# Kernel optimization log

Hardware: AMD Instinct MI355X
Metric: run time of the kernel (lower is better)

## Reference

```python
import jax, jax.numpy as jnp
import numpy as np

DT = 0.5
DX = 0.01
MU_UP = 4e-05
PAD = 3  # 7x7 kernel // 2

_LAP = np.array([[0, 0, 0, 2, 0, 0, 0],
                 [0, 0, 0, -27, 0, 0, 0],
                 [0, 0, 0, 270, 0, 0, 0],
                 [2, -27, 270, -980, 270, -27, 2],
                 [0, 0, 0, 270, 0, 0, 0],
                 [0, 0, 0, -27, 0, 0, 0],
                 [0, 0, 0, 2, 0, 0, 0]], dtype=np.float32)
LAP_W = jnp.asarray(_LAP / (DX * DX) / 180.0)[None, None]  # [1,1,7,7]


def _laplace(x):
    # x: [B,1,H,W]; circular padding then valid conv (matches padding_mode='circular')
    xp = jnp.pad(x, ((0, 0), (0, 0), (PAD, PAD), (PAD, PAD)), mode='wrap')
    return jax.lax.conv_general_dilated(xp, LAP_W, (1, 1), 'VALID',
                                        dimension_numbers=('NCHW', 'OIHW', 'NCHW'))


def setup_inputs() -> dict:
    key = jax.random.key(0)
    ks = jax.random.split(key, 7)
    h = jax.random.uniform(ks[0], (16, 2, 1024, 1024), dtype=jnp.float32)
    CA = jax.random.uniform(ks[1], (), dtype=jnp.float32) - 0.5  # ~ -rand()+0.5
    CB = jax.random.uniform(ks[2], (), dtype=jnp.float32) - 0.5
    NA = -jax.random.uniform(ks[3], (), dtype=jnp.float32)
    NB = jax.random.uniform(ks[4], (), dtype=jnp.float32)
    f = 0.1 * jax.random.uniform(ks[5], (), dtype=jnp.float32)
    k = 0.1 * jax.random.uniform(ks[6], (), dtype=jnp.float32)
    return {"h": h, "CA": CA, "CB": CB, "NA": NA, "NB": NB, "f": f, "k": k}


def reference(h, CA, CB, NA, NB, f, k):
    mu_u = MU_UP * jax.nn.sigmoid(CA)
    mu_v = MU_UP * jax.nn.sigmoid(CB)

    def f_rhs(u, v):
        uv2 = u * v * v
        f_u = mu_u * _laplace(u) + NA * uv2 + f * (1.0 - u)
        f_v = mu_v * _laplace(v) + NB * uv2 - (k + f) * v
        return f_u, f_v

    u0 = h[:, 0:1]
    v0 = h[:, 1:2]
    k1_u, k1_v = f_rhs(u0, v0)
    k2_u, k2_v = f_rhs(u0 + k1_u * (DT / 2.0), v0 + k1_v * (DT / 2.0))
    k3_u, k3_v = f_rhs(u0 + k2_u * (DT / 2.0), v0 + k2_v * (DT / 2.0))
    k4_u, k4_v = f_rhs(u0 + k3_u * DT, v0 + k3_v * DT)
    u_next = u0 + DT * (k1_u + 2.0 * k2_u + 2.0 * k3_u + k4_u) / 6.0
    v_next = v0 + DT * (k1_v + 2.0 * k2_v + 2.0 * k3_v + k4_v) / 6.0
    return jnp.concatenate((u_next, v_next), axis=1)
```

## Files before the change

### kernel.cpp

```cpp
#include <hip/hip_runtime.h>


typedef float f2 __attribute__((ext_vector_type(2)));
typedef float f4 __attribute__((ext_vector_type(4)));

#define HROWS 64
#define NT    512
#define STEPS (HROWS + 24)

#define W0 ((-980.0f / 1e-4f) / 180.0f)
#define W1 ((  270.0f / 1e-4f) / 180.0f)
#define W2 (( -27.0f / 1e-4f) / 180.0f)
#define W3 ((   2.0f / 1e-4f) / 180.0f)

__device__ __forceinline__ f2 sp(float s) { f2 r; r.x = s; r.y = s; return r; }
__device__ __forceinline__ f2 pfma(float s, f2 a, f2 c) {
    return __builtin_elementwise_fma(sp(s), a, c);
}
__device__ __forceinline__ f2 lo2(f4 a) { return __builtin_shufflevector(a, a, 0, 1); }
__device__ __forceinline__ f2 hi2(f4 a) { return __builtin_shufflevector(a, a, 2, 3); }
__device__ __forceinline__ f4 cat(f2 a, f2 b) { return __builtin_shufflevector(a, b, 0, 1, 2, 3); }

struct Hq  { f2 m2, m1, p1, p2; };
struct Hq4 { f4 m2, m1, p1, p2; };

__device__ __forceinline__ Hq4 rdq4(const f4* __restrict__ L,
                                    int xm2, int xm1, int xp1, int xp2) {
    Hq4 q;
    q.m2 = L[xm2]; q.m1 = L[xm1]; q.p1 = L[xp1]; q.p2 = L[xp2];
    return q;
}

__device__ __forceinline__ void evalp7(f2 w0, f2 w1, f2 w2, f2 w3, f2 w4,
                                       f2 w5, f2 w6, const Hq& q,
                                       f2& lap, f2& ctr)
{
    ctr = w3;
    f2 vp = pfma(W1, w2 + w4, pfma(W2, w1 + w5, sp(W3) * (w0 + w6)));
    f2 m1 = __builtin_shufflevector(q.m1, ctr, 1, 2);
    f2 p1 = __builtin_shufflevector(ctr, q.p1, 1, 2);
    f2 m3 = __builtin_shufflevector(q.m2, q.m1, 1, 2);
    f2 p3 = __builtin_shufflevector(q.p1, q.p2, 1, 2);
    f2 hp = pfma(W1, m1 + p1, pfma(W2, q.m1 + q.p1, sp(W3) * (m3 + p3)));
    lap = pfma(W0, ctr, hp + vp);
}

__global__ __launch_bounds__(NT, 1) void rcnn_rk4_march(
    const float* __restrict__ h,
    const float* __restrict__ pCA, const float* __restrict__ pCB,
    const float* __restrict__ pNA, const float* __restrict__ pNB,
    const float* __restrict__ pf,  const float* __restrict__ pk,
    float* __restrict__ out)
{
    __shared__ f4 S[4][4][NT];

    const int tid = threadIdx.x;
    const int Y0  = blockIdx.x * HROWS;
    const int b   = blockIdx.z;

    const float NA = pNA[0], NB = pNB[0];
    const float ff = pf[0];
    const float kpf = pk[0] + pf[0];
    const float mu_u = 4e-5f / (1.0f + expf(-pCA[0]));
    const float mu_v = 4e-5f / (1.0f + expf(-pCB[0]));

    const size_t baseU = (size_t)b * 2u * 1048576u;
    const size_t baseV = baseU + 1048576u;
    const float* hU = h + baseU + 2 * tid;
    const float* hV = h + baseV + 2 * tid;
    float* oU = out + baseU + 2 * tid;
    float* oV = out + baseV + 2 * tid;

    const int xm2 = (tid - 2) & 511;
    const int xm1 = (tid - 1) & 511;
    const int xp1 = (tid + 1) & 511;
    const int xp2 = (tid + 2) & 511;

    f2 Uu[8], Uv[8], Du[8], Dv[8];
    f2 Y1u[8], Y1v[8], Y2u[8], Y2v[8], Y3u[8], Y3v[8];
    f2 ACu[8], ACv[8];

    const f2 z = sp(0.0f);
    #pragma unroll
    for (int j = 0; j < 8; ++j) {
        Uu[j]=z; Uv[j]=z; Du[j]=z; Dv[j]=z;
        Y1u[j]=z; Y1v[j]=z; Y2u[j]=z; Y2v[j]=z; Y3u[j]=z; Y3v[j]=z;
        ACu[j]=z; ACv[j]=z;
    }

    f2 pAu, pAv, pBu, pBv;
    {
        int r0 = (Y0 - 12) & 1023;
        int r1 = (Y0 - 11) & 1023;
        pAu = *(const f2*)(hU + (size_t)r0 * 1024);
        pAv = *(const f2*)(hV + (size_t)r0 * 1024);
        pBu = *(const f2*)(hU + (size_t)r1 * 1024);
        pBv = *(const f2*)(hV + (size_t)r1 * 1024);
    }

#define STEP(c, G1, G2, G3, G4, tb_)                                          \
  {                                                                           \
    const int t_ = (tb_) + (c);                                               \
                             \
    Du[(c)&7] = Uu[((c)+3)&7]; Dv[(c)&7] = Uv[((c)+3)&7];                     \
                                             \
    Uu[(c)&7] = ((c)&1) ? pBu : pAu;                                          \
    Uv[(c)&7] = ((c)&1) ? pBv : pAv;                                          \
                          \
    S[0][(c)&3][tid] = cat(Uu[((c)+7)&7], Uv[((c)+7)&7]);                     \
                                             \
    {                                                                         \
      int yn = (Y0 - 10 + t_) & 1023;                                         \
      f2 au = *(const f2*)(hU + (size_t)yn * 1024);                           \
      f2 av = *(const f2*)(hV + (size_t)yn * 1024);                           \
      if ((c)&1) { pBu = au; pBv = av; } else { pAu = au; pAv = av; }         \
    }                                                                         \
    if (G1) {                                         \
      Hq4 q = rdq4(&S[0][((c)+2)&3][0], xm2, xm1, xp1, xp2);                  \
      Hq qu = { lo2(q.m2), lo2(q.m1), lo2(q.p1), lo2(q.p2) };                 \
      Hq qv = { hi2(q.m2), hi2(q.m1), hi2(q.p1), hi2(q.p2) };                 \
      f2 lU, cU, lV, cV;                                                      \
      evalp7(Uu[((c)+2)&7], Uu[((c)+3)&7], Uu[((c)+4)&7], Uu[((c)+5)&7],      \
             Uu[((c)+6)&7], Uu[((c)+7)&7], Uu[(c)&7], qu, lU, cU);            \
      evalp7(Uv[((c)+2)&7], Uv[((c)+3)&7], Uv[((c)+4)&7], Uv[((c)+5)&7],      \
             Uv[((c)+6)&7], Uv[((c)+7)&7], Uv[(c)&7], qv, lV, cV);            \
      f2 uv2 = cU * cV * cV;                                                  \
      f2 kU = pfma(mu_u, lU, pfma(NA, uv2, pfma(-ff, cU, sp(ff))));           \
      f2 kV = pfma(mu_v, lV, pfma(NB, uv2, sp(-kpf) * cV));                   \
      Y1u[(c)&7] = pfma(0.25f, kU, cU);                                       \
      Y1v[(c)&7] = pfma(0.25f, kV, cV);                                       \
      S[1][(c)&3][tid] = cat(Y1u[((c)+7)&7], Y1v[((c)+7)&7]);                 \
    }                                                                         \
    if (G2) {                               \
      Hq4 q = rdq4(&S[1][((c)+2)&3][0], xm2, xm1, xp1, xp2);                  \
      Hq qu = { lo2(q.m2), lo2(q.m1), lo2(q.p1), lo2(q.p2) };                 \
      Hq qv = { hi2(q.m2), hi2(q.m1), hi2(q.p1), hi2(q.p2) };                 \
      f2 lU, cU, lV, cV;                                                      \
      evalp7(Y1u[((c)+2)&7], Y1u[((c)+3)&7], Y1u[((c)+4)&7], Y1u[((c)+5)&7],  \
             Y1u[((c)+6)&7], Y1u[((c)+7)&7], Y1u[(c)&7], qu, lU, cU);         \
      evalp7(Y1v[((c)+2)&7], Y1v[((c)+3)&7], Y1v[((c)+4)&7], Y1v[((c)+5)&7],  \
             Y1v[((c)+6)&7], Y1v[((c)+7)&7], Y1v[(c)&7], qv, lV, cV);         \
      f2 uv2 = cU * cV * cV;                                                  \
      f2 kU = pfma(mu_u, lU, pfma(NA, uv2, pfma(-ff, cU, sp(ff))));           \
      f2 kV = pfma(mu_v, lV, pfma(NB, uv2, sp(-kpf) * cV));                   \
      f2 bu = Du[((c)+7)&7], bv = Dv[((c)+7)&7];                \
      f2 nu = pfma(0.25f, kU, bu), nv = pfma(0.25f, kV, bv);                  \
      Y2u[(c)&7] = nu; Y2v[(c)&7] = nv;                                       \
      f2 aU = pfma(4.0f, Y1u[((c)+5)&7], sp(8.0f) * nu);                      \
      f2 aV = pfma(4.0f, Y1v[((c)+5)&7], sp(8.0f) * nv);                      \
      ACu[(c)&7] = pfma(-4.0f, bu, aU);                                       \
      ACv[(c)&7] = pfma(-4.0f, bv, aV);                                       \
      S[2][(c)&3][tid] = cat(Y2u[((c)+7)&7], Y2v[((c)+7)&7]);                 \
    }                                                                         \
    if (G3) {                                         \
      Hq4 q = rdq4(&S[2][((c)+2)&3][0], xm2, xm1, xp1, xp2);                  \
      Hq qu = { lo2(q.m2), lo2(q.m1), lo2(q.p1), lo2(q.p2) };                 \
      Hq qv = { hi2(q.m2), hi2(q.m1), hi2(q.p1), hi2(q.p2) };                 \
      f2 lU, cU, lV, cV;                                                      \
      evalp7(Y2u[((c)+2)&7], Y2u[((c)+3)&7], Y2u[((c)+4)&7], Y2u[((c)+5)&7],  \
             Y2u[((c)+6)&7], Y2u[((c)+7)&7], Y2u[(c)&7], qu, lU, cU);         \
      evalp7(Y2v[((c)+2)&7], Y2v[((c)+3)&7], Y2v[((c)+4)&7], Y2v[((c)+5)&7],  \
             Y2v[((c)+6)&7], Y2v[((c)+7)&7], Y2v[(c)&7], qv, lV, cV);         \
      f2 uv2 = cU * cV * cV;                                                  \
      f2 kU = pfma(mu_u, lU, pfma(NA, uv2, pfma(-ff, cU, sp(ff))));           \
      f2 kV = pfma(mu_v, lV, pfma(NB, uv2, sp(-kpf) * cV));                   \
      Y3u[(c)&7] = pfma(0.5f, kU, Du[((c)+4)&7]);               \
      Y3v[(c)&7] = pfma(0.5f, kV, Dv[((c)+4)&7]);                             \
      S[3][(c)&3][tid] = cat(Y3u[((c)+7)&7], Y3v[((c)+7)&7]);                 \
    }                                                                         \
    if (G4) {                         \
      Hq4 q = rdq4(&S[3][((c)+2)&3][0], xm2, xm1, xp1, xp2);                  \
      Hq qu = { lo2(q.m2), lo2(q.m1), lo2(q.p1), lo2(q.p2) };                 \
      Hq qv = { hi2(q.m2), hi2(q.m1), hi2(q.p1), hi2(q.p2) };                 \
      f2 lU, cU4, lV, cV4;                                                    \
      evalp7(Y3u[((c)+2)&7], Y3u[((c)+3)&7], Y3u[((c)+4)&7], Y3u[((c)+5)&7],  \
             Y3u[((c)+6)&7], Y3u[((c)+7)&7], Y3u[(c)&7], qu, lU, cU4);        \
      evalp7(Y3v[((c)+2)&7], Y3v[((c)+3)&7], Y3v[((c)+4)&7], Y3v[((c)+5)&7],  \
             Y3v[((c)+6)&7], Y3v[((c)+7)&7], Y3v[(c)&7], qv, lV, cV4);        \
      f2 uv2 = cU4 * cV4 * cV4;                                               \
      f2 kU = pfma(mu_u, lU, pfma(NA, uv2, pfma(-ff, cU4, sp(ff))));          \
      f2 kV = pfma(mu_v, lV, pfma(NB, uv2, sp(-kpf) * cV4));                  \
      f2 sU = pfma(4.0f, cU4, kU) + ACu[((c)+2)&7];             \
      f2 sV = pfma(4.0f, cV4, kV) + ACv[((c)+2)&7];                           \
      f2 oUq = sp(1.0f / 12.0f) * sU;                                         \
      f2 oVq = sp(1.0f / 12.0f) * sV;                                         \
      int yS = Y0 + t_ - 24;                                                  \
      *(f2*)(oU + (size_t)yS * 1024) = oUq;                                   \
      *(f2*)(oV + (size_t)yS * 1024) = oVq;                                   \
    }                                                                         \
    if ((c) & 1) {                                                            \
      asm volatile("s_waitcnt lgkmcnt(0)" ::: "memory");                      \
      __builtin_amdgcn_s_barrier();                                           \
    }                                                                         \
  }

    STEP(0,0,0,0,0, 0) STEP(1,0,0,0,0, 0) STEP(2,0,0,0,0, 0) STEP(3,0,0,0,0, 0)
    STEP(4,0,0,0,0, 0) STEP(5,0,0,0,0, 0) STEP(6,1,0,0,0, 0) STEP(7,1,0,0,0, 0)

    STEP(0,1,0,0,0, 8) STEP(1,1,0,0,0, 8) STEP(2,1,0,0,0, 8) STEP(3,1,0,0,0, 8)
    STEP(4,1,1,0,0, 8) STEP(5,1,1,0,0, 8) STEP(6,1,1,0,0, 8) STEP(7,1,1,0,0, 8)

    STEP(0,1,1,0,0,16) STEP(1,1,1,0,0,16) STEP(2,1,1,1,0,16) STEP(3,1,1,1,0,16)
    STEP(4,1,1,1,0,16) STEP(5,1,1,1,0,16) STEP(6,1,1,1,0,16) STEP(7,1,1,1,0,16)

    #pragma unroll 1
    for (int tb = 24; tb < STEPS; tb += 8) {
        STEP(0,1,1,1,1,tb) STEP(1,1,1,1,1,tb) STEP(2,1,1,1,1,tb) STEP(3,1,1,1,1,tb)
        STEP(4,1,1,1,1,tb) STEP(5,1,1,1,1,tb) STEP(6,1,1,1,1,tb) STEP(7,1,1,1,1,tb)
    }
#undef STEP
}

extern "C" void kernel_launch(void* const* d_in, const int* in_sizes, int n_in,
                              void* d_out, int out_size, void* d_ws, size_t ws_size,
                              hipStream_t stream) {
    const float* h   = (const float*)d_in[0];
    const float* pCA = (const float*)d_in[1];
    const float* pCB = (const float*)d_in[2];
    const float* pNA = (const float*)d_in[3];
    const float* pNB = (const float*)d_in[4];
    const float* pf  = (const float*)d_in[5];
    const float* pk  = (const float*)d_in[6];
    float* outp = (float*)d_out;

    dim3 grid(1024 / HROWS, 1, 16);
    dim3 block(NT);
    rcnn_rk4_march<<<grid, block, 0, stream>>>(h, pCA, pCB, pNA, pNB, pf, pk, outp);
}
```

Measured before the change: 90.44 us.

## Read stage-1 horizontal halo from global memory instead of shared memory

The first RK stage no longer writes the input rows to shared memory and reads neighbours back. Each thread instead loads unaligned float4 windows around its columns straight from global (served from cache), two rows ahead, with special handling for the circular wrap at the row ends. This frees one of the four LDS stage buffers and removes one LDS write/read round per row. In exchange it adds extra global loads, more registers for the prefetch buffers, and per-thread edge branches.

```diff
diff --git a/kernel.cpp b/kernel.cpp
--- a/kernel.cpp
+++ b/kernel.cpp
@@ -3,6 +3,7 @@
 
 typedef float f2 __attribute__((ext_vector_type(2)));
 typedef float f4 __attribute__((ext_vector_type(4)));
+typedef float f4a __attribute__((ext_vector_type(4), aligned(4)));
 
 #define HROWS 64
 #define NT    512
@@ -31,18 +32,25 @@
     return q;
 }
 
+__device__ __forceinline__ void evalp7x(f2 w0, f2 w1, f2 w2, f2 w3, f2 w4,
+                                        f2 w5, f2 w6, f2 m1, f2 p1,
+                                        float am3, float bp3,
+                                        f2& lap, f2& ctr)
+{
+    ctr = w3;
+    f2 vp = pfma(W1, w2 + w4, pfma(W2, w1 + w5, sp(W3) * (w0 + w6)));
+    f2 m1q; m1q.x = m1.y;  m1q.y = ctr.x;
+    f2 p1q; p1q.x = ctr.y; p1q.y = p1.x;
+    f2 m3q; m3q.x = am3;   m3q.y = m1.x;
+    f2 p3q; p3q.x = p1.y;  p3q.y = bp3;
+    f2 hp = pfma(W1, m1q + p1q, pfma(W2, m1 + p1, sp(W3) * (m3q + p3q)));
+    lap = pfma(W0, ctr, hp + vp);
+}
 __device__ __forceinline__ void evalp7(f2 w0, f2 w1, f2 w2, f2 w3, f2 w4,
                                        f2 w5, f2 w6, const Hq& q,
                                        f2& lap, f2& ctr)
 {
-    ctr = w3;
-    f2 vp = pfma(W1, w2 + w4, pfma(W2, w1 + w5, sp(W3) * (w0 + w6)));
-    f2 m1 = __builtin_shufflevector(q.m1, ctr, 1, 2);
-    f2 p1 = __builtin_shufflevector(ctr, q.p1, 1, 2);
-    f2 m3 = __builtin_shufflevector(q.m2, q.m1, 1, 2);
-    f2 p3 = __builtin_shufflevector(q.p1, q.p2, 1, 2);
-    f2 hp = pfma(W1, m1 + p1, pfma(W2, q.m1 + q.p1, sp(W3) * (m3 + p3)));
-    lap = pfma(W0, ctr, hp + vp);
+    evalp7x(w0, w1, w2, w3, w4, w5, w6, q.m1, q.p1, q.m2.y, q.p2.x, lap, ctr);
 }
 
 __global__ __launch_bounds__(NT, 1) void rcnn_rk4_march(
@@ -52,7 +60,7 @@
     const float* __restrict__ pf,  const float* __restrict__ pk,
     float* __restrict__ out)
 {
-    __shared__ f4 S[4][4][NT];
+    __shared__ f4 S[3][4][NT];
 
     const int tid = threadIdx.x;
     const int Y0  = blockIdx.x * HROWS;
@@ -66,8 +74,10 @@
 
     const size_t baseU = (size_t)b * 2u * 1048576u;
     const size_t baseV = baseU + 1048576u;
-    const float* hU = h + baseU + 2 * tid;
-    const float* hV = h + baseV + 2 * tid;
+    const float* hUr = h + baseU;
+    const float* hVr = h + baseV;
+    const float* hU = hUr + 2 * tid;
+    const float* hV = hVr + 2 * tid;
     float* oU = out + baseU + 2 * tid;
     float* oV = out + baseV + 2 * tid;
 
@@ -75,10 +85,16 @@
     const int xm1 = (tid - 1) & 511;
     const int xp1 = (tid + 1) & 511;
     const int xp2 = (tid + 2) & 511;
+    const int mc  = max(2 * tid - 3, 0);
+    const int pc  = min(2 * tid + 2, 1020);
+    const bool edgew = (tid < 64) || (tid >= 448);
 
     f2 Uu[8], Uv[8], Du[8], Dv[8];
     f2 Y1u[8], Y1v[8], Y2u[8], Y2v[8], Y3u[8], Y3v[8];
     f2 ACu[8], ACv[8];
+
+    f4 mqU[2], pqU[2], mqV[2], pqV[2];
+    f4 wLoU[2], wHiU[2], wLoV[2], wHiV[2];
 
     const f2 z = sp(0.0f);
     #pragma unroll
@@ -86,6 +102,12 @@
         Uu[j]=z; Uv[j]=z; Du[j]=z; Dv[j]=z;
         Y1u[j]=z; Y1v[j]=z; Y2u[j]=z; Y2v[j]=z; Y3u[j]=z; Y3v[j]=z;
         ACu[j]=z; ACv[j]=z;
+    }
+    const f4 z4 = {0.f,0.f,0.f,0.f};
+    #pragma unroll
+    for (int j = 0; j < 2; ++j) {
+        mqU[j]=z4; pqU[j]=z4; mqV[j]=z4; pqV[j]=z4;
+        wLoU[j]=z4; wHiU[j]=z4; wLoV[j]=z4; wHiV[j]=z4;
     }
 
     f2 pAu, pAv, pBu, pBv;
@@ -106,8 +128,6 @@
                                              \
     Uu[(c)&7] = ((c)&1) ? pBu : pAu;                                          \
     Uv[(c)&7] = ((c)&1) ? pBv : pAv;                                          \
-                          \
-    S[0][(c)&3][tid] = cat(Uu[((c)+7)&7], Uv[((c)+7)&7]);                     \
                                              \
     {                                                                         \
       int yn = (Y0 - 10 + t_) & 1023;                                         \
@@ -115,24 +135,65 @@
       f2 av = *(const f2*)(hV + (size_t)yn * 1024);                           \
       if ((c)&1) { pBu = au; pBv = av; } else { pAu = au; pAv = av; }         \
     }                                                                         \
-    if (G1) {                                         \
-      Hq4 q = rdq4(&S[0][((c)+2)&3][0], xm2, xm1, xp1, xp2);                  \
-      Hq qu = { lo2(q.m2), lo2(q.m1), lo2(q.p1), lo2(q.p2) };                 \
-      Hq qv = { hi2(q.m2), hi2(q.m1), hi2(q.p1), hi2(q.p2) };                 \
+          \
+    {                                                                         \
+      int yr = (Y0 - 14 + t_) & 1023;                                         \
+      const float* rU = hUr + (size_t)yr * 1024;                              \
+      const float* rV = hVr + (size_t)yr * 1024;                              \
+      mqU[(c)&1] = *(const f4a*)(rU + mc);                                    \
+      pqU[(c)&1] = *(const f4a*)(rU + pc);                                    \
+      mqV[(c)&1] = *(const f4a*)(rV + mc);                                    \
+      pqV[(c)&1] = *(const f4a*)(rV + pc);                                    \
+      if (edgew) {                                                            \
+        wLoU[(c)&1] = *(const f4*)(rU);                                       \
+        wHiU[(c)&1] = *(const f4*)(rU + 1020);                                \
+        wLoV[(c)&1] = *(const f4*)(rV);                                       \
+        wHiV[(c)&1] = *(const f4*)(rV + 1020);                                \
+      }                                                                       \
+    }                                                                         \
+    if (G1) {   \
+      f4 mqu = mqU[((c)+1)&1], pqu = pqU[((c)+1)&1];                          \
+      f4 mqv = mqV[((c)+1)&1], pqv = pqV[((c)+1)&1];                          \
+      f2 m1u; m1u.x = mqu.y; m1u.y = mqu.z;  float am3u = mqu.x;              \
+      f2 p1u; p1u.x = pqu.x; p1u.y = pqu.y;  float bp3u = pqu.z;              \
+      f2 m1v; m1v.x = mqv.y; m1v.y = mqv.z;  float am3v = mqv.x;              \
+      f2 p1v; p1v.x = pqv.x; p1v.y = pqv.y;  float bp3v = pqv.z;              \
+      if (tid < 2) {                                                          \
+        f4 whu = wHiU[((c)+1)&1], whv = wHiV[((c)+1)&1];                      \
+        if (tid == 0) {                                                       \
+          am3u = whu.y; m1u.x = whu.z; m1u.y = whu.w;                         \
+          am3v = whv.y; m1v.x = whv.z; m1v.y = whv.w;                         \
+        } else {                                                              \
+          am3u = whu.w; m1u.x = mqu.x; m1u.y = mqu.y;                         \
+          am3v = whv.w; m1v.x = mqv.x; m1v.y = mqv.y;                         \
+        }                                                                     \
+      }                                                                       \
+      if (tid >= 510) {                                                       \
+        f4 wlu = wLoU[((c)+1)&1], wlv = wLoV[((c)+1)&1];                      \
+        if (tid == 510) {                                                     \
+          p1u.x = pqu.z; p1u.y = pqu.w; bp3u = wlu.x;                         \
+          p1v.x = pqv.z; p1v.y = pqv.w; bp3v = wlv.x;                         \
+        } else {                                                              \
+          p1u.x = wlu.x; p1u.y = wlu.y; bp3u = wlu.z;                         \
+          p1v.x = wlv.x; p1v.y = wlv.y; bp3v = wlv.z;                         \
+        }                                                                     \
+      }                                                                       \
       f2 lU, cU, lV, cV;                                                      \
-      evalp7(Uu[((c)+2)&7], Uu[((c)+3)&7], Uu[((c)+4)&7], Uu[((c)+5)&7],      \
-             Uu[((c)+6)&7], Uu[((c)+7)&7], Uu[(c)&7], qu, lU, cU);            \
-      evalp7(Uv[((c)+2)&7], Uv[((c)+3)&7], Uv[((c)+4)&7], Uv[((c)+5)&7],      \
-             Uv[((c)+6)&7], Uv[((c)+7)&7], Uv[(c)&7], qv, lV, cV);            \
+      evalp7x(Uu[((c)+2)&7], Uu[((c)+3)&7], Uu[((c)+4)&7], Uu[((c)+5)&7],     \
+              Uu[((c)+6)&7], Uu[((c)+7)&7], Uu[(c)&7],                        \
+              m1u, p1u, am3u, bp3u, lU, cU);                                  \
+      evalp7x(Uv[((c)+2)&7], Uv[((c)+3)&7], Uv[((c)+4)&7], Uv[((c)+5)&7],     \
+              Uv[((c)+6)&7], Uv[((c)+7)&7], Uv[(c)&7],                        \
+              m1v, p1v, am3v, bp3v, lV, cV);                                  \
       f2 uv2 = cU * cV * cV;                                                  \
       f2 kU = pfma(mu_u, lU, pfma(NA, uv2, pfma(-ff, cU, sp(ff))));           \
       f2 kV = pfma(mu_v, lV, pfma(NB, uv2, sp(-kpf) * cV));                   \
       Y1u[(c)&7] = pfma(0.25f, kU, cU);                                       \
       Y1v[(c)&7] = pfma(0.25f, kV, cV);                                       \
-      S[1][(c)&3][tid] = cat(Y1u[((c)+7)&7], Y1v[((c)+7)&7]);                 \
+      S[0][(c)&3][tid] = cat(Y1u[((c)+7)&7], Y1v[((c)+7)&7]);                 \
     }                                                                         \
     if (G2) {                               \
-      Hq4 q = rdq4(&S[1][((c)+2)&3][0], xm2, xm1, xp1, xp2);                  \
+      Hq4 q = rdq4(&S[0][((c)+2)&3][0], xm2, xm1, xp1, xp2);                  \
       Hq qu = { lo2(q.m2), lo2(q.m1), lo2(q.p1), lo2(q.p2) };                 \
       Hq qv = { hi2(q.m2), hi2(q.m1), hi2(q.p1), hi2(q.p2) };                 \
       f2 lU, cU, lV, cV;                                                      \
@@ -150,10 +211,10 @@
       f2 aV = pfma(4.0f, Y1v[((c)+5)&7], sp(8.0f) * nv);                      \
       ACu[(c)&7] = pfma(-4.0f, bu, aU);                                       \
       ACv[(c)&7] = pfma(-4.0f, bv, aV);                                       \
-      S[2][(c)&3][tid] = cat(Y2u[((c)+7)&7], Y2v[((c)+7)&7]);                 \
+      S[1][(c)&3][tid] = cat(Y2u[((c)+7)&7], Y2v[((c)+7)&7]);                 \
     }                                                                         \
     if (G3) {                                         \
-      Hq4 q = rdq4(&S[2][((c)+2)&3][0], xm2, xm1, xp1, xp2);                  \
+      Hq4 q = rdq4(&S[1][((c)+2)&3][0], xm2, xm1, xp1, xp2);                  \
       Hq qu = { lo2(q.m2), lo2(q.m1), lo2(q.p1), lo2(q.p2) };                 \
       Hq qv = { hi2(q.m2), hi2(q.m1), hi2(q.p1), hi2(q.p2) };                 \
       f2 lU, cU, lV, cV;                                                      \
@@ -166,10 +227,10 @@
       f2 kV = pfma(mu_v, lV, pfma(NB, uv2, sp(-kpf) * cV));                   \
       Y3u[(c)&7] = pfma(0.5f, kU, Du[((c)+4)&7]);               \
       Y3v[(c)&7] = pfma(0.5f, kV, Dv[((c)+4)&7]);                             \
-      S[3][(c)&3][tid] = cat(Y3u[((c)+7)&7], Y3v[((c)+7)&7]);                 \
+      S[2][(c)&3][tid] = cat(Y3u[((c)+7)&7], Y3v[((c)+7)&7]);                 \
     }                                                                         \
     if (G4) {                         \
-      Hq4 q = rdq4(&S[3][((c)+2)&3][0], xm2, xm1, xp1, xp2);                  \
+      Hq4 q = rdq4(&S[2][((c)+2)&3][0], xm2, xm1, xp1, xp2);                  \
       Hq qu = { lo2(q.m2), lo2(q.m1), lo2(q.p1), lo2(q.p2) };                 \
       Hq qv = { hi2(q.m2), hi2(q.m1), hi2(q.p1), hi2(q.p2) };                 \
       f2 lU, cU4, lV, cV4;                                                    \
```

Result: slower. 116.3 us (+28.6%).
